# Optimization experiments

Hardware: AMD Instinct MI355X
Metric: run time of the kernel (lower is better)

The kernel has to match this reference:

```python
import jax, jax.numpy as jnp
import numpy as np

EPS = 0.01          # halting threshold eps
MAX_STEPS = 16      # static cap on the data-dependent while-loop (bias=1.0 halts in ~2 steps)


def setup_inputs() -> dict:
    key = jax.random.key(0)
    ks = jax.random.split(key, 10)
    I, H, O = 4096, 4096, 4096
    sc = 1.0 / np.sqrt(H)
    u = lambda k, shape: jax.random.uniform(k, shape, jnp.float32, -sc, sc)
    return {
        "x": jax.random.normal(ks[0], (I,), jnp.float32),
        "s": jax.random.normal(ks[1], (H,), jnp.float32) * 0.1,
        "W_ih": u(ks[2], (H, 1 + I)),   # nn.RNN weight_ih_l0
        "b_ih": u(ks[3], (H,)),
        "W_hh": u(ks[4], (H, H)),       # nn.RNN weight_hh_l0
        "b_hh": u(ks[5], (H,)),
        "w_halt": u(ks[6], (1, H)),     # fc_halt.weight
        "b_halt": jnp.array([1.0], jnp.float32),  # fc_halt.bias init per module
        "W_out": u(ks[7], (O, H)),      # fc_output.weight
        "b_out": u(ks[8], (O,)),
    }


def reference(x, s, W_ih, b_ih, W_hh, b_hh, w_halt, b_halt, W_out, b_out):
    # x1 = [1, x] for the first step, x0 = [0, x] for subsequent steps
    x0 = jnp.concatenate([jnp.zeros((1,), x.dtype), x])
    x1 = jnp.concatenate([jnp.ones((1,), x.dtype), x])

    def step(h, t):
        xin = jnp.where(t == 0, x1, x0)
        # torch nn.RNN (tanh) cell: h' = tanh(W_ih x + b_ih + W_hh h + b_hh)
        h = jnp.tanh(W_ih @ xin + b_ih + W_hh @ h + b_hh)
        out = W_out @ h + b_out                 # fc_output
        p = jax.nn.sigmoid(w_halt @ h + b_halt)[0]  # fc_halt -> sigmoid
        return h, (h, out, p)

    _, (hs, outs, ps) = jax.lax.scan(step, s, jnp.arange(MAX_STEPS))
    # accumulated halting probability; loop stops at first step with cum >= 1-eps.
    cum = jnp.cumsum(ps)
    crossed = cum >= 1.0 - EPS
    # Binarize: only the first crossing step gets 1 (cum is strictly increasing,
    # and the original while-loop exits there), so mv with the binarized vector
    # selects outputs/states at step N, and ponder = sum(1 - bin) = N.
    N = jnp.where(jnp.any(crossed), jnp.argmax(crossed), MAX_STEPS - 1)
    output = outs[N]
    s_new = hs[N]
    ponder = N.astype(x.dtype)
    return output, s_new, ponder
```

## Files before the change

### kernel.cpp

```cpp
#include <hip/hip_runtime.h>

static constexpr int   H           = 4096;
static constexpr int   TPB         = 256;
static constexpr int   NB          = H / 4;
static constexpr int   MAX_STEPS   = 16;
static constexpr float EPS         = 0.01f;
static constexpr int   SLOTS       = 64;
static constexpr int   SLOT_STRIDE = 32;

static constexpr int WS_V0   = 0;
static constexpr int WS_WIH0 = H;
static constexpr int WS_TOT  = 2 * H;
static constexpr int WS_PART = 2 * H + 32;
static constexpr int WS_H    = WS_PART + MAX_STEPS * SLOTS * SLOT_STRIDE;

__device__ __forceinline__ float wave_reduce(float v) {
    #pragma unroll
    for (int off = 32; off > 0; off >>= 1) v += __shfl_down(v, off);
    return v;
}
__device__ __forceinline__ float sigmoidf(float z) { return 1.f / (1.f + __expf(-z)); }

__global__ void __launch_bounds__(TPB)
k_init(const float* __restrict__ x, const float* __restrict__ s,
       const float* __restrict__ Wih, const float* __restrict__ bih,
       const float* __restrict__ bhh, float* __restrict__ ws)
{
    __shared__ float xs[H];
    const int tid = threadIdx.x, lane = tid & 63, wave = tid >> 6;
    const int row = blockIdx.x * 4 + wave;

    for (int i = tid; i < H / 4; i += TPB)
        ((float4*)xs)[i] = ((const float4*)x)[i];
    __syncthreads();

    const long long off0 = (long long)row * (H + 1) + 1;
    const int a = (int)((4 - (off0 & 3)) & 3);
    float acc = 0.f;
    if (lane < a) acc += Wih[off0 + lane] * xs[lane];
    const int nvec = (H - a) >> 2;
    const float4* wv = (const float4*)(Wih + off0 + a);
    for (int i = lane; i < nvec; i += 64) {
        float4 w  = wv[i];
        const int e = a + i * 4;
        acc = fmaf(w.x, xs[e],     acc);
        acc = fmaf(w.y, xs[e + 1], acc);
        acc = fmaf(w.z, xs[e + 2], acc);
        acc = fmaf(w.w, xs[e + 3], acc);
    }
    const int tail  = (H - a) & 3;
    const int tbase = a + nvec * 4;
    if (lane < tail) acc += Wih[off0 + tbase + lane] * xs[tbase + lane];
    acc = wave_reduce(acc);
    if (lane == 0) {
        ws[WS_V0 + row]   = acc + bih[row] + bhh[row];
        ws[WS_WIH0 + row] = Wih[(long long)row * (H + 1)];
    }

    const int gid = blockIdx.x * TPB + tid;
    if (gid < H) ws[WS_H + gid] = s[gid];
    if (gid < 32 + MAX_STEPS * SLOTS * SLOT_STRIDE)
        ws[WS_TOT + gid] = 0.f;
}

__global__ void __launch_bounds__(TPB, 4)
k_step(int t, const float* __restrict__ Whh, const float* __restrict__ whalt,
       const float* __restrict__ bhalt, float* __restrict__ ws)
{
    const float bh = bhalt[0];

    float cum = 0.f;
    for (int j = 0; j < t - 1; ++j) {
        cum += sigmoidf(ws[WS_TOT + j] + bh);
        if (cum >= 1.f - EPS) return;
    }
    if (t >= 1) {
        float sj = 0.f;
        const float* p = ws + WS_PART + (size_t)(t - 1) * (SLOTS * SLOT_STRIDE);
        #pragma unroll
        for (int g = 0; g < SLOTS; ++g) sj += p[g * SLOT_STRIDE];
        if (threadIdx.x == 0) ws[WS_TOT + (t - 1)] = sj;
        cum += sigmoidf(sj + bh);
        if (cum >= 1.f - EPS) return;
    }

    __shared__ float hs[H];
    __shared__ float hred[4];
    const int tid = threadIdx.x, lane = tid & 63, wave = tid >> 6;
    const float* hin  = ws + WS_H + (size_t)(t & 1) * H;
    float*       hout = ws + WS_H + (size_t)((t + 1) & 1) * H;
    for (int i = tid; i < H / 4; i += TPB)
        ((float4*)hs)[i] = ((const float4*)hin)[i];
    __syncthreads();

    const int row = blockIdx.x * 4 + wave;
    const float4* Wr = (const float4*)(Whh + (size_t)row * H);
    float4 w[16];
    #pragma unroll
    for (int it = 0; it < 16; ++it) w[it] = Wr[it * 64 + lane];
    float acc = 0.f;
    #pragma unroll
    for (int it = 0; it < 16; ++it) {
        float4 hv = ((const float4*)hs)[it * 64 + lane];
        acc = fmaf(w[it].x, hv.x, acc);
        acc = fmaf(w[it].y, hv.y, acc);
        acc = fmaf(w[it].z, hv.z, acc);
        acc = fmaf(w[it].w, hv.w, acc);
    }
    acc = wave_reduce(acc);
    if (lane == 0) {
        float pre  = acc + ws[WS_V0 + row] + (t == 0 ? ws[WS_WIH0 + row] : 0.f);
        float hval = tanhf(pre);
        hout[row]  = hval;
        hred[wave] = whalt[row] * hval;
    }
    __syncthreads();
    if (tid == 0) {
        float v = hred[0] + hred[1] + hred[2] + hred[3];
        atomicAdd(&ws[WS_PART + (size_t)t * (SLOTS * SLOT_STRIDE)
                      + (blockIdx.x & (SLOTS - 1)) * SLOT_STRIDE], v);
    }
}

__global__ void __launch_bounds__(TPB, 4)
k_final(const float* __restrict__ Wout, const float* __restrict__ bout,
        const float* __restrict__ bhalt, float* __restrict__ ws,
        float* __restrict__ out)
{
    const float bh = bhalt[0];
    float cum = 0.f;
    int N = MAX_STEPS - 1;
    for (int j = 0; j < MAX_STEPS; ++j) {
        float sj;
        if (j < MAX_STEPS - 1) sj = ws[WS_TOT + j];
        else {
            sj = 0.f;
            const float* p = ws + WS_PART + (size_t)(MAX_STEPS - 1) * (SLOTS * SLOT_STRIDE);
            #pragma unroll
            for (int g = 0; g < SLOTS; ++g) sj += p[g * SLOT_STRIDE];
        }
        cum += sigmoidf(sj + bh);
        if (cum >= 1.f - EPS) { N = j; break; }
    }

    __shared__ float hs[H];
    const float* hN = ws + WS_H + (size_t)((N + 1) & 1) * H;
    const int tid = threadIdx.x, lane = tid & 63, wave = tid >> 6;
    for (int i = tid; i < H / 4; i += TPB)
        ((float4*)hs)[i] = ((const float4*)hN)[i];
    __syncthreads();

    const int row = blockIdx.x * 4 + wave;
    const float4* Wr = (const float4*)(Wout + (size_t)row * H);
    float4 w[16];
    #pragma unroll
    for (int it = 0; it < 16; ++it) w[it] = Wr[it * 64 + lane];
    float acc = 0.f;
    #pragma unroll
    for (int it = 0; it < 16; ++it) {
        float4 hv = ((const float4*)hs)[it * 64 + lane];
        acc = fmaf(w[it].x, hv.x, acc);
        acc = fmaf(w[it].y, hv.y, acc);
        acc = fmaf(w[it].z, hv.z, acc);
        acc = fmaf(w[it].w, hv.w, acc);
    }
    acc = wave_reduce(acc);
    if (lane == 0) {
        out[row]     = acc + bout[row];
        out[H + row] = hs[row];
        if (row == 0) out[2 * H] = (float)N;
    }
}

extern "C" void kernel_launch(void* const* d_in, const int* in_sizes, int n_in,
                              void* d_out, int out_size, void* d_ws, size_t ws_size,
                              hipStream_t stream) {
    const float* x     = (const float*)d_in[0];
    const float* s     = (const float*)d_in[1];
    const float* Wih   = (const float*)d_in[2];
    const float* bih   = (const float*)d_in[3];
    const float* Whh   = (const float*)d_in[4];
    const float* bhh   = (const float*)d_in[5];
    const float* whalt = (const float*)d_in[6];
    const float* bhalt = (const float*)d_in[7];
    const float* Wout  = (const float*)d_in[8];
    const float* bout  = (const float*)d_in[9];
    float* out = (float*)d_out;
    float* ws  = (float*)d_ws;

    k_init<<<NB, TPB, 0, stream>>>(x, s, Wih, bih, bhh, ws);
    for (int t = 0; t < MAX_STEPS; ++t)
        k_step<<<NB, TPB, 0, stream>>>(t, Whh, whalt, bhalt, ws);
    k_final<<<NB, TPB, 0, stream>>>(Wout, bout, bhalt, ws, out);
}
```

Baseline: 257.6 us.

## Fuse init, recurrent steps and output into one cooperative persistent kernel

Replaces the chain of 18 kernel launches (init, 16 steps, final) with a single cooperative kernel of 256 blocks x 1024 threads that uses grid.sync between recurrent steps. Each block computes the halting sum deterministically from per-block partials and breaks out of the loop once the threshold is reached. This removes per-launch overhead and the early-exit kernels that ran after halting. The multi-kernel path is kept as a fallback when cooperative launch is unavailable. The cost is grid-wide barriers and only 256 blocks, so fewer loads are in flight per step.

```diff
diff --git a/kernel.cpp b/kernel.cpp
--- a/kernel.cpp
+++ b/kernel.cpp
@@ -1,18 +1,11 @@
 #include <hip/hip_runtime.h>
-
-static constexpr int   H           = 4096;
-static constexpr int   TPB         = 256;
-static constexpr int   NB          = H / 4;
-static constexpr int   MAX_STEPS   = 16;
-static constexpr float EPS         = 0.01f;
-static constexpr int   SLOTS       = 64;
-static constexpr int   SLOT_STRIDE = 32;
-
-static constexpr int WS_V0   = 0;
-static constexpr int WS_WIH0 = H;
-static constexpr int WS_TOT  = 2 * H;
-static constexpr int WS_PART = 2 * H + 32;
-static constexpr int WS_H    = WS_PART + MAX_STEPS * SLOTS * SLOT_STRIDE;
+#include <hip/hip_cooperative_groups.h>
+
+namespace cg = cooperative_groups;
+
+static constexpr int   H         = 4096;
+static constexpr int   MAX_STEPS = 16;
+static constexpr float EPS       = 0.01f;
 
 __device__ __forceinline__ float wave_reduce(float v) {
     #pragma unroll
@@ -20,6 +13,144 @@
     return v;
 }
 __device__ __forceinline__ float sigmoidf(float z) { return 1.f / (1.f + __expf(-z)); }
+
+static constexpr int TPB_C = 1024;
+static constexpr int NB_C  = 256;
+static constexpr int CWS_H    = 0;
+static constexpr int CWS_PART = 2 * H;
+
+__global__ void __launch_bounds__(TPB_C, 4)
+k_fused(const float* __restrict__ x,     const float* __restrict__ s,
+        const float* __restrict__ Wih,   const float* __restrict__ bih,
+        const float* __restrict__ Whh,   const float* __restrict__ bhh,
+        const float* __restrict__ whalt, const float* __restrict__ bhalt,
+        const float* __restrict__ Wout,  const float* __restrict__ bout,
+        float* __restrict__ ws,          float* __restrict__ out)
+{
+    cg::grid_group grid = cg::this_grid();
+    __shared__ float sh[H];
+    __shared__ float hred[16];
+    const int tid = threadIdx.x, lane = tid & 63, wave = tid >> 6;
+    const int row = blockIdx.x * 16 + wave;
+    float* wsH  = ws + CWS_H;
+    float* part = ws + CWS_PART;
+    const float bh = bhalt[0];
+
+    for (int i = tid; i < H / 4; i += TPB_C)
+        ((float4*)sh)[i] = ((const float4*)x)[i];
+    __syncthreads();
+
+    const long long off0 = (long long)row * (H + 1) + 1;
+    const int a = (int)((4 - (off0 & 3)) & 3);
+    float acc = 0.f;
+    if (lane < a) acc += Wih[off0 + lane] * sh[lane];
+    const int nvec = (H - a) >> 2;
+    const float4* wv = (const float4*)(Wih + off0 + a);
+    for (int i = lane; i < nvec; i += 64) {
+        float4 w  = wv[i];
+        const int e = a + i * 4;
+        acc = fmaf(w.x, sh[e],     acc);
+        acc = fmaf(w.y, sh[e + 1], acc);
+        acc = fmaf(w.z, sh[e + 2], acc);
+        acc = fmaf(w.w, sh[e + 3], acc);
+    }
+    const int tail  = (H - a) & 3;
+    const int tbase = a + nvec * 4;
+    if (lane < tail) acc += Wih[off0 + tbase + lane] * sh[tbase + lane];
+    acc = wave_reduce(acc);
+    float v0 = 0.f, wih0 = 0.f;
+    if (lane == 0) {
+        v0   = acc + bih[row] + bhh[row];
+        wih0 = Wih[(long long)row * (H + 1)];
+    }
+    __syncthreads();
+
+    int   N   = MAX_STEPS - 1;
+    float cum = 0.f;
+    for (int t = 0; t < MAX_STEPS; ++t) {
+        const float* hin = (t == 0) ? s : (wsH + (size_t)(t & 1) * H);
+        for (int i = tid; i < H / 4; i += TPB_C)
+            ((float4*)sh)[i] = ((const float4*)hin)[i];
+        __syncthreads();
+
+        const float4* Wr = (const float4*)(Whh + (size_t)row * H);
+        float4 w[16];
+        #pragma unroll
+        for (int it = 0; it < 16; ++it) w[it] = Wr[it * 64 + lane];
+        float a2 = 0.f;
+        #pragma unroll
+        for (int it = 0; it < 16; ++it) {
+            float4 hv = ((const float4*)sh)[it * 64 + lane];
+            a2 = fmaf(w[it].x, hv.x, a2);
+            a2 = fmaf(w[it].y, hv.y, a2);
+            a2 = fmaf(w[it].z, hv.z, a2);
+            a2 = fmaf(w[it].w, hv.w, a2);
+        }
+        a2 = wave_reduce(a2);
+        if (lane == 0) {
+            float pre  = a2 + v0 + (t == 0 ? wih0 : 0.f);
+            float hval = tanhf(pre);
+            wsH[(size_t)((t + 1) & 1) * H + row] = hval;
+            hred[wave] = whalt[row] * hval;
+        }
+        __syncthreads();
+        if (tid == 0) {
+            float v = 0.f;
+            #pragma unroll
+            for (int j2 = 0; j2 < 16; ++j2) v += hred[j2];
+            part[t * NB_C + blockIdx.x] = v;
+        }
+        __threadfence();
+        grid.sync();
+
+        float sl = (tid < NB_C) ? part[t * NB_C + tid] : 0.f;
+        sl = wave_reduce(sl);
+        if (lane == 0) hred[wave] = sl;
+        __syncthreads();
+        float sj = 0.f;
+        #pragma unroll
+        for (int j2 = 0; j2 < 16; ++j2) sj += hred[j2];
+        cum += sigmoidf(sj + bh);
+        __syncthreads();
+        if (cum >= 1.f - EPS) { N = t; break; }
+    }
+
+    const float* hN = wsH + (size_t)((N + 1) & 1) * H;
+    for (int i = tid; i < H / 4; i += TPB_C)
+        ((float4*)sh)[i] = ((const float4*)hN)[i];
+    __syncthreads();
+
+    const float4* Wr = (const float4*)(Wout + (size_t)row * H);
+    float4 w[16];
+    #pragma unroll
+    for (int it = 0; it < 16; ++it) w[it] = Wr[it * 64 + lane];
+    float a3 = 0.f;
+    #pragma unroll
+    for (int it = 0; it < 16; ++it) {
+        float4 hv = ((const float4*)sh)[it * 64 + lane];
+        a3 = fmaf(w[it].x, hv.x, a3);
+        a3 = fmaf(w[it].y, hv.y, a3);
+        a3 = fmaf(w[it].z, hv.z, a3);
+        a3 = fmaf(w[it].w, hv.w, a3);
+    }
+    a3 = wave_reduce(a3);
+    if (lane == 0) {
+        out[row]     = a3 + bout[row];
+        out[H + row] = sh[row];
+        if (row == 0) out[2 * H] = (float)N;
+    }
+}
+
+static constexpr int TPB         = 256;
+static constexpr int NB          = H / 4;
+static constexpr int SLOTS       = 64;
+static constexpr int SLOT_STRIDE = 32;
+
+static constexpr int FWS_V0   = 0;
+static constexpr int FWS_WIH0 = H;
+static constexpr int FWS_TOT  = 2 * H;
+static constexpr int FWS_PART = 2 * H + 32;
+static constexpr int FWS_H    = FWS_PART + MAX_STEPS * SLOTS * SLOT_STRIDE;
 
 __global__ void __launch_bounds__(TPB)
 k_init(const float* __restrict__ x, const float* __restrict__ s,
@@ -53,14 +184,14 @@
     if (lane < tail) acc += Wih[off0 + tbase + lane] * xs[tbase + lane];
     acc = wave_reduce(acc);
     if (lane == 0) {
-        ws[WS_V0 + row]   = acc + bih[row] + bhh[row];
-        ws[WS_WIH0 + row] = Wih[(long long)row * (H + 1)];
+        ws[FWS_V0 + row]   = acc + bih[row] + bhh[row];
+        ws[FWS_WIH0 + row] = Wih[(long long)row * (H + 1)];
     }
 
     const int gid = blockIdx.x * TPB + tid;
-    if (gid < H) ws[WS_H + gid] = s[gid];
+    if (gid < H) ws[FWS_H + gid] = s[gid];
     if (gid < 32 + MAX_STEPS * SLOTS * SLOT_STRIDE)
-        ws[WS_TOT + gid] = 0.f;
+        ws[FWS_TOT + gid] = 0.f;
 }
 
 __global__ void __launch_bounds__(TPB, 4)
@@ -71,15 +202,15 @@
 
     float cum = 0.f;
     for (int j = 0; j < t - 1; ++j) {
-        cum += sigmoidf(ws[WS_TOT + j] + bh);
+        cum += sigmoidf(ws[FWS_TOT + j] + bh);
         if (cum >= 1.f - EPS) return;
     }
     if (t >= 1) {
         float sj = 0.f;
-        const float* p = ws + WS_PART + (size_t)(t - 1) * (SLOTS * SLOT_STRIDE);
+        const float* p = ws + FWS_PART + (size_t)(t - 1) * (SLOTS * SLOT_STRIDE);
         #pragma unroll
         for (int g = 0; g < SLOTS; ++g) sj += p[g * SLOT_STRIDE];
-        if (threadIdx.x == 0) ws[WS_TOT + (t - 1)] = sj;
+        if (threadIdx.x == 0) ws[FWS_TOT + (t - 1)] = sj;
         cum += sigmoidf(sj + bh);
         if (cum >= 1.f - EPS) return;
     }
@@ -87,8 +218,8 @@
     __shared__ float hs[H];
     __shared__ float hred[4];
     const int tid = threadIdx.x, lane = tid & 63, wave = tid >> 6;
-    const float* hin  = ws + WS_H + (size_t)(t & 1) * H;
-    float*       hout = ws + WS_H + (size_t)((t + 1) & 1) * H;
+    const float* hin  = ws + FWS_H + (size_t)(t & 1) * H;
+    float*       hout = ws + FWS_H + (size_t)((t + 1) & 1) * H;
     for (int i = tid; i < H / 4; i += TPB)
         ((float4*)hs)[i] = ((const float4*)hin)[i];
     __syncthreads();
@@ -109,7 +240,7 @@
     }
     acc = wave_reduce(acc);
     if (lane == 0) {
-        float pre  = acc + ws[WS_V0 + row] + (t == 0 ? ws[WS_WIH0 + row] : 0.f);
+        float pre  = acc + ws[FWS_V0 + row] + (t == 0 ? ws[FWS_WIH0 + row] : 0.f);
         float hval = tanhf(pre);
         hout[row]  = hval;
         hred[wave] = whalt[row] * hval;
@@ -117,7 +248,7 @@
     __syncthreads();
     if (tid == 0) {
         float v = hred[0] + hred[1] + hred[2] + hred[3];
-        atomicAdd(&ws[WS_PART + (size_t)t * (SLOTS * SLOT_STRIDE)
+        atomicAdd(&ws[FWS_PART + (size_t)t * (SLOTS * SLOT_STRIDE)
                       + (blockIdx.x & (SLOTS - 1)) * SLOT_STRIDE], v);
     }
 }
@@ -132,10 +263,10 @@
     int N = MAX_STEPS - 1;
     for (int j = 0; j < MAX_STEPS; ++j) {
         float sj;
-        if (j < MAX_STEPS - 1) sj = ws[WS_TOT + j];
+        if (j < MAX_STEPS - 1) sj = ws[FWS_TOT + j];
         else {
             sj = 0.f;
-            const float* p = ws + WS_PART + (size_t)(MAX_STEPS - 1) * (SLOTS * SLOT_STRIDE);
+            const float* p = ws + FWS_PART + (size_t)(MAX_STEPS - 1) * (SLOTS * SLOT_STRIDE);
             #pragma unroll
             for (int g = 0; g < SLOTS; ++g) sj += p[g * SLOT_STRIDE];
         }
@@ -144,7 +275,7 @@
     }
 
     __shared__ float hs[H];
-    const float* hN = ws + WS_H + (size_t)((N + 1) & 1) * H;
+    const float* hN = ws + FWS_H + (size_t)((N + 1) & 1) * H;
     const int tid = threadIdx.x, lane = tid & 63, wave = tid >> 6;
     for (int i = tid; i < H / 4; i += TPB)
         ((float4*)hs)[i] = ((const float4*)hN)[i];
@@ -188,6 +319,25 @@
     float* out = (float*)d_out;
     float* ws  = (float*)d_ws;
 
+    static int use_coop = -1;
+    if (use_coop < 0) {
+        int dev = 0;  (void)hipGetDevice(&dev);
+        int coop = 0; (void)hipDeviceGetAttribute(&coop, hipDeviceAttributeCooperativeLaunch, dev);
+        int ncu = 0;  (void)hipDeviceGetAttribute(&ncu, hipDeviceAttributeMultiprocessorCount, dev);
+        int maxb = 0;
+        (void)hipOccupancyMaxActiveBlocksPerMultiprocessor(&maxb, k_fused, TPB_C, 0);
+        use_coop = (coop != 0 && (long long)maxb * (long long)ncu >= NB_C) ? 1 : 0;
+    }
+
+    if (use_coop == 1) {
+        void* args[] = { &x, &s, &Wih, &bih, &Whh, &bhh, &whalt, &bhalt,
+                         &Wout, &bout, &ws, &out };
+        hipError_t e = hipLaunchCooperativeKernel((const void*)k_fused, dim3(NB_C),
+                                                  dim3(TPB_C), args, 0, stream);
+        if (e == hipSuccess) return;
+        use_coop = 0;
+    }
+
     k_init<<<NB, TPB, 0, stream>>>(x, s, Wih, bih, bhh, ws);
     for (int t = 0; t < MAX_STEPS; ++t)
         k_step<<<NB, TPB, 0, stream>>>(t, Whh, whalt, bhalt, ws);
```

After: 258.4 us. No clear change (+0.3%).

## Fuse recurrent steps into three kernels with redundant halting and grid barrier

Applied to the files above, without the earlier changes.

Replaces the init kernel, the 16 per-step launches and the final kernel with three kernels. kA computes the input projection and the first W_hh·s in parallel. kB has every block rebuild h1 and compute the halting sum itself, then applies either W_out or the next W_hh. kC runs any remaining steps in a persistent loop with a global atomic barrier. This removes about 15 launches, the atomic partial-sum slots and the serial halting scans. The cost is a full redundant h/halt reduction in every block, and kC depends on all 1024 blocks being co-resident for the spin barrier.

```diff
diff --git a/kernel.cpp b/kernel.cpp
--- a/kernel.cpp
+++ b/kernel.cpp
@@ -1,18 +1,19 @@
 #include <hip/hip_runtime.h>
 
-static constexpr int   H           = 4096;
-static constexpr int   TPB         = 256;
-static constexpr int   NB          = H / 4;
-static constexpr int   MAX_STEPS   = 16;
-static constexpr float EPS         = 0.01f;
-static constexpr int   SLOTS       = 64;
-static constexpr int   SLOT_STRIDE = 32;
+static constexpr int   H         = 4096;
+static constexpr int   MAX_STEPS = 16;
+static constexpr float EPS       = 0.01f;
+
+static constexpr int TPB  = 256;
+static constexpr int NB   = H / 4;
+static constexpr int NB_A = 2 * NB;
 
 static constexpr int WS_V0   = 0;
-static constexpr int WS_WIH0 = H;
-static constexpr int WS_TOT  = 2 * H;
-static constexpr int WS_PART = 2 * H + 32;
-static constexpr int WS_H    = WS_PART + MAX_STEPS * SLOTS * SLOT_STRIDE;
+static constexpr int WS_PRE1 = H;
+static constexpr int WS_AH0  = 2 * H;
+static constexpr int WS_HRAW = 3 * H;
+static constexpr int WS_CTRL = 5 * H;
+static constexpr int WS_CNT  = 5 * H + 2;
 
 __device__ __forceinline__ float wave_reduce(float v) {
     #pragma unroll
@@ -21,80 +22,8 @@
 }
 __device__ __forceinline__ float sigmoidf(float z) { return 1.f / (1.f + __expf(-z)); }
 
-__global__ void __launch_bounds__(TPB)
-k_init(const float* __restrict__ x, const float* __restrict__ s,
-       const float* __restrict__ Wih, const float* __restrict__ bih,
-       const float* __restrict__ bhh, float* __restrict__ ws)
-{
-    __shared__ float xs[H];
-    const int tid = threadIdx.x, lane = tid & 63, wave = tid >> 6;
-    const int row = blockIdx.x * 4 + wave;
-
-    for (int i = tid; i < H / 4; i += TPB)
-        ((float4*)xs)[i] = ((const float4*)x)[i];
-    __syncthreads();
-
-    const long long off0 = (long long)row * (H + 1) + 1;
-    const int a = (int)((4 - (off0 & 3)) & 3);
-    float acc = 0.f;
-    if (lane < a) acc += Wih[off0 + lane] * xs[lane];
-    const int nvec = (H - a) >> 2;
-    const float4* wv = (const float4*)(Wih + off0 + a);
-    for (int i = lane; i < nvec; i += 64) {
-        float4 w  = wv[i];
-        const int e = a + i * 4;
-        acc = fmaf(w.x, xs[e],     acc);
-        acc = fmaf(w.y, xs[e + 1], acc);
-        acc = fmaf(w.z, xs[e + 2], acc);
-        acc = fmaf(w.w, xs[e + 3], acc);
-    }
-    const int tail  = (H - a) & 3;
-    const int tbase = a + nvec * 4;
-    if (lane < tail) acc += Wih[off0 + tbase + lane] * xs[tbase + lane];
-    acc = wave_reduce(acc);
-    if (lane == 0) {
-        ws[WS_V0 + row]   = acc + bih[row] + bhh[row];
-        ws[WS_WIH0 + row] = Wih[(long long)row * (H + 1)];
-    }
-
-    const int gid = blockIdx.x * TPB + tid;
-    if (gid < H) ws[WS_H + gid] = s[gid];
-    if (gid < 32 + MAX_STEPS * SLOTS * SLOT_STRIDE)
-        ws[WS_TOT + gid] = 0.f;
-}
-
-__global__ void __launch_bounds__(TPB, 4)
-k_step(int t, const float* __restrict__ Whh, const float* __restrict__ whalt,
-       const float* __restrict__ bhalt, float* __restrict__ ws)
-{
-    const float bh = bhalt[0];
-
-    float cum = 0.f;
-    for (int j = 0; j < t - 1; ++j) {
-        cum += sigmoidf(ws[WS_TOT + j] + bh);
-        if (cum >= 1.f - EPS) return;
-    }
-    if (t >= 1) {
-        float sj = 0.f;
-        const float* p = ws + WS_PART + (size_t)(t - 1) * (SLOTS * SLOT_STRIDE);
-        #pragma unroll
-        for (int g = 0; g < SLOTS; ++g) sj += p[g * SLOT_STRIDE];
-        if (threadIdx.x == 0) ws[WS_TOT + (t - 1)] = sj;
-        cum += sigmoidf(sj + bh);
-        if (cum >= 1.f - EPS) return;
-    }
-
-    __shared__ float hs[H];
-    __shared__ float hred[4];
-    const int tid = threadIdx.x, lane = tid & 63, wave = tid >> 6;
-    const float* hin  = ws + WS_H + (size_t)(t & 1) * H;
-    float*       hout = ws + WS_H + (size_t)((t + 1) & 1) * H;
-    for (int i = tid; i < H / 4; i += TPB)
-        ((float4*)hs)[i] = ((const float4*)hin)[i];
-    __syncthreads();
-
-    const int row = blockIdx.x * 4 + wave;
-    const float4* Wr = (const float4*)(Whh + (size_t)row * H);
+__device__ __forceinline__ float dot_row16(const float4* __restrict__ Wr,
+                                           const float* __restrict__ hs, int lane) {
     float4 w[16];
     #pragma unroll
     for (int it = 0; it < 16; ++it) w[it] = Wr[it * 64 + lane];
@@ -107,63 +36,168 @@
         acc = fmaf(w[it].z, hv.z, acc);
         acc = fmaf(w[it].w, hv.w, acc);
     }
+    return acc;
+}
+
+__global__ void __launch_bounds__(TPB, 8)
+kA(const float* __restrict__ x,   const float* __restrict__ s,
+   const float* __restrict__ Wih, const float* __restrict__ bih,
+   const float* __restrict__ Whh, const float* __restrict__ bhh,
+   float* __restrict__ ws)
+{
+    __shared__ float vs[H];
+    const int tid = threadIdx.x, lane = tid & 63, wave = tid >> 6;
+    const bool ih = (blockIdx.x < (unsigned)NB);
+    const int row = (ih ? blockIdx.x : blockIdx.x - NB) * 4 + wave;
+
+    const float* src = ih ? x : s;
+    for (int i = tid; i < H / 4; i += TPB)
+        ((float4*)vs)[i] = ((const float4*)src)[i];
+    if (blockIdx.x == 0 && tid < 16) ((int*)(ws + WS_CNT))[tid] = 0;
+    __syncthreads();
+
+    if (ih) {
+        const size_t row_off = (size_t)row * (H + 1);
+        const size_t start   = row_off + 1;
+        const int    m       = (int)(start & 3);
+        const float4* wv = (const float4*)(Wih + (start - m));
+        float4 w[16];
+        #pragma unroll
+        for (int it = 0; it < 16; ++it) w[it] = wv[it * 64 + lane];
+        float acc = 0.f;
+        {
+            const int kb = lane * 4 - m;
+            if (kb + 0 >= 0) acc = fmaf(w[0].x, vs[kb + 0], acc);
+            if (kb + 1 >= 0) acc = fmaf(w[0].y, vs[kb + 1], acc);
+            if (kb + 2 >= 0) acc = fmaf(w[0].z, vs[kb + 2], acc);
+            if (kb + 3 >= 0) acc = fmaf(w[0].w, vs[kb + 3], acc);
+        }
+        #pragma unroll
+        for (int it = 1; it < 16; ++it) {
+            const int kb = it * 256 + lane * 4 - m;
+            acc = fmaf(w[it].x, vs[kb + 0], acc);
+            acc = fmaf(w[it].y, vs[kb + 1], acc);
+            acc = fmaf(w[it].z, vs[kb + 2], acc);
+            acc = fmaf(w[it].w, vs[kb + 3], acc);
+        }
+        if (lane < m)
+            acc += Wih[start + 4096 - m + lane] * vs[4096 - m + lane];
+        acc = wave_reduce(acc);
+        if (lane == 0) {
+            const float v0 = acc + bih[row] + bhh[row];
+            ws[WS_V0   + row] = v0;
+            ws[WS_PRE1 + row] = v0 + Wih[row_off];
+        }
+    } else {
+        float acc = dot_row16((const float4*)(Whh + (size_t)row * H), vs, lane);
+        acc = wave_reduce(acc);
+        if (lane == 0) ws[WS_AH0 + row] = acc;
+    }
+}
+
+__global__ void __launch_bounds__(TPB, 4)
+kB(const float* __restrict__ Whh,   const float* __restrict__ Wout,
+   const float* __restrict__ whalt, const float* __restrict__ bhalt,
+   const float* __restrict__ bout,  float* __restrict__ ws,
+   float* __restrict__ out)
+{
+    __shared__ float hs[H];
+    __shared__ float red[4];
+    const int tid = threadIdx.x, lane = tid & 63, wave = tid >> 6;
+    const int row = blockIdx.x * 4 + wave;
+
+    float psum = 0.f;
+    for (int i = tid; i < H / 4; i += TPB) {
+        float4 p  = ((const float4*)(ws + WS_PRE1))[i];
+        float4 a  = ((const float4*)(ws + WS_AH0))[i];
+        float4 wl = ((const float4*)whalt)[i];
+        float4 h;
+        h.x = tanhf(p.x + a.x); h.y = tanhf(p.y + a.y);
+        h.z = tanhf(p.z + a.z); h.w = tanhf(p.w + a.w);
+        ((float4*)hs)[i] = h;
+        psum = fmaf(wl.x, h.x, psum); psum = fmaf(wl.y, h.y, psum);
+        psum = fmaf(wl.z, h.z, psum); psum = fmaf(wl.w, h.w, psum);
+    }
+    psum = wave_reduce(psum);
+    if (lane == 0) red[wave] = psum;
+    __syncthreads();
+    const float cum0 = sigmoidf(red[0] + red[1] + red[2] + red[3] + bhalt[0]);
+    const bool halted0 = (cum0 >= 1.f - EPS);
+    if (blockIdx.x == 0 && tid == 0) {
+        ws[WS_CTRL]     = halted0 ? 1.f : 0.f;
+        ws[WS_CTRL + 1] = cum0;
+    }
+
+    const float* W = halted0 ? Wout : Whh;
+    float acc = dot_row16((const float4*)(W + (size_t)row * H), hs, lane);
     acc = wave_reduce(acc);
     if (lane == 0) {
-        float pre  = acc + ws[WS_V0 + row] + (t == 0 ? ws[WS_WIH0 + row] : 0.f);
-        float hval = tanhf(pre);
-        hout[row]  = hval;
-        hred[wave] = whalt[row] * hval;
-    }
-    __syncthreads();
-    if (tid == 0) {
-        float v = hred[0] + hred[1] + hred[2] + hred[3];
-        atomicAdd(&ws[WS_PART + (size_t)t * (SLOTS * SLOT_STRIDE)
-                      + (blockIdx.x & (SLOTS - 1)) * SLOT_STRIDE], v);
-    }
-}
-
-__global__ void __launch_bounds__(TPB, 4)
-k_final(const float* __restrict__ Wout, const float* __restrict__ bout,
-        const float* __restrict__ bhalt, float* __restrict__ ws,
-        float* __restrict__ out)
+        if (halted0) {
+            out[row]     = acc + bout[row];
+            out[H + row] = hs[row];
+            if (row == 0) out[2 * H] = 0.f;
+        } else {
+            ws[WS_HRAW + H + row] = acc;
+        }
+    }
+}
+
+__device__ __forceinline__ void gbarrier(int* cnt) {
+    __syncthreads();
+    if (threadIdx.x == 0) {
+        __threadfence();
+        atomicAdd(cnt, 1);
+        while (atomicAdd(cnt, 0) < NB) __builtin_amdgcn_s_sleep(8);
+        __threadfence();
+    }
+    __syncthreads();
+}
+
+__global__ void __launch_bounds__(TPB, 8)
+kC(const float* __restrict__ Whh,   const float* __restrict__ Wout,
+   const float* __restrict__ whalt, const float* __restrict__ bhalt,
+   const float* __restrict__ bout,  float* __restrict__ ws,
+   float* __restrict__ out)
 {
+    if (ws[WS_CTRL] > 0.5f) return;
+    __shared__ float hs[H];
+    __shared__ float red[4];
+    const int tid = threadIdx.x, lane = tid & 63, wave = tid >> 6;
+    const int row = blockIdx.x * 4 + wave;
     const float bh = bhalt[0];
-    float cum = 0.f;
+
+    float cum = ws[WS_CTRL + 1];
     int N = MAX_STEPS - 1;
-    for (int j = 0; j < MAX_STEPS; ++j) {
-        float sj;
-        if (j < MAX_STEPS - 1) sj = ws[WS_TOT + j];
-        else {
-            sj = 0.f;
-            const float* p = ws + WS_PART + (size_t)(MAX_STEPS - 1) * (SLOTS * SLOT_STRIDE);
-            #pragma unroll
-            for (int g = 0; g < SLOTS; ++g) sj += p[g * SLOT_STRIDE];
-        }
-        cum += sigmoidf(sj + bh);
-        if (cum >= 1.f - EPS) { N = j; break; }
-    }
-
-    __shared__ float hs[H];
-    const float* hN = ws + WS_H + (size_t)((N + 1) & 1) * H;
-    const int tid = threadIdx.x, lane = tid & 63, wave = tid >> 6;
-    for (int i = tid; i < H / 4; i += TPB)
-        ((float4*)hs)[i] = ((const float4*)hN)[i];
-    __syncthreads();
-
-    const int row = blockIdx.x * 4 + wave;
-    const float4* Wr = (const float4*)(Wout + (size_t)row * H);
-    float4 w[16];
-    #pragma unroll
-    for (int it = 0; it < 16; ++it) w[it] = Wr[it * 64 + lane];
-    float acc = 0.f;
-    #pragma unroll
-    for (int it = 0; it < 16; ++it) {
-        float4 hv = ((const float4*)hs)[it * 64 + lane];
-        acc = fmaf(w[it].x, hv.x, acc);
-        acc = fmaf(w[it].y, hv.y, acc);
-        acc = fmaf(w[it].z, hv.z, acc);
-        acc = fmaf(w[it].w, hv.w, acc);
-    }
+    int cur = 1;
+    for (int t = 1; t < MAX_STEPS; ++t) {
+        float psum = 0.f;
+        const float4* v0v = (const float4*)(ws + WS_V0);
+        const float4* rv  = (const float4*)(ws + WS_HRAW + cur * H);
+        for (int i = tid; i < H / 4; i += TPB) {
+            float4 v  = v0v[i];
+            float4 r  = rv[i];
+            float4 wl = ((const float4*)whalt)[i];
+            float4 h;
+            h.x = tanhf(v.x + r.x); h.y = tanhf(v.y + r.y);
+            h.z = tanhf(v.z + r.z); h.w = tanhf(v.w + r.w);
+            ((float4*)hs)[i] = h;
+            psum = fmaf(wl.x, h.x, psum); psum = fmaf(wl.y, h.y, psum);
+            psum = fmaf(wl.z, h.z, psum); psum = fmaf(wl.w, h.w, psum);
+        }
+        psum = wave_reduce(psum);
+        if (lane == 0) red[wave] = psum;
+        __syncthreads();
+        cum += sigmoidf(red[0] + red[1] + red[2] + red[3] + bh);
+        if (cum >= 1.f - EPS || t == MAX_STEPS - 1) { N = t; break; }
+
+        float acc = dot_row16((const float4*)(Whh + (size_t)row * H), hs, lane);
+        acc = wave_reduce(acc);
+        if (lane == 0) ws[WS_HRAW + (cur ^ 1) * H + row] = acc;
+        gbarrier(((int*)(ws + WS_CNT)) + t);
+        cur ^= 1;
+    }
+
+    float acc = dot_row16((const float4*)(Wout + (size_t)row * H), hs, lane);
     acc = wave_reduce(acc);
     if (lane == 0) {
         out[row]     = acc + bout[row];
@@ -188,8 +222,7 @@
     float* out = (float*)d_out;
     float* ws  = (float*)d_ws;
 
-    k_init<<<NB, TPB, 0, stream>>>(x, s, Wih, bih, bhh, ws);
-    for (int t = 0; t < MAX_STEPS; ++t)
-        k_step<<<NB, TPB, 0, stream>>>(t, Whh, whalt, bhalt, ws);
-    k_final<<<NB, TPB, 0, stream>>>(Wout, bout, bhalt, ws, out);
-}
+    kA<<<NB_A, TPB, 0, stream>>>(x, s, Wih, bih, Whh, bhh, ws);
+    kB<<<NB,   TPB, 0, stream>>>(Whh, Wout, whalt, bhalt, bout, ws, out);
+    kC<<<NB,   TPB, 0, stream>>>(Whh, Wout, whalt, bhalt, bout, ws, out);
+}
```

Measured after the change: 240.5 us. -6.6%, faster.
